# Kernel optimization log

Measured on AMD Instinct MI355X. Metric: run time of the kernel, lower is better.

Reference implementation:

```python
import jax, jax.numpy as jnp
import numpy as np

L = 2        # NUM_DECODER_LAYERS
D = 512      # D_MODEL == ENCODER_EMBEDDING_DIM == DECODER_EMBEDDING_DIM == DECODER_HIDDEN_DIM
T = 32       # max_trg_len (greedy decode steps)
SOS = 1      # SPECIAL_TOKENS.index('[SOS]'), PAD assumed 0


def setup_inputs() -> dict:
    key = jax.random.key(0)
    ks = jax.random.split(key, 12)
    Vin, Vout, B, S = 32000, 32000, 32, 512
    s = 0.02
    src = jax.random.randint(ks[0], (B, S), 0, Vin)
    src_emb_table = jax.random.normal(ks[1], (Vin, D), dtype=jnp.float32) * s
    trg_emb_table = (jax.random.normal(ks[2], (Vout, D), dtype=jnp.float32) * s).at[0].set(0.0)  # padding_idx=0
    Wih = jax.random.normal(ks[3], (L, 4 * D, D), dtype=jnp.float32) * s
    Whh = jax.random.normal(ks[4], (L, 4 * D, D), dtype=jnp.float32) * s
    bih = jnp.zeros((L, 4 * D), jnp.float32)
    bhh = jnp.zeros((L, 4 * D), jnp.float32)
    Wfc = jax.random.normal(ks[5], (D, D), dtype=jnp.float32) * s      # Decoder.fc_out (hid_dim -> hid_dim)
    bfc = jnp.zeros((D,), jnp.float32)
    Wh2o = jax.random.normal(ks[6], (D, 2 * D), dtype=jnp.float32) * s  # hidden_to_out
    bh2o = jnp.zeros((D,), jnp.float32)
    bout = jnp.zeros((Vout,), jnp.float32)                              # out_layer bias (weight tied to trg_emb_table)
    return dict(src=src, src_emb_table=src_emb_table, trg_emb_table=trg_emb_table,
                Wih=Wih, Whh=Whh, bih=bih, bhh=bhh, Wfc=Wfc, bfc=bfc,
                Wh2o=Wh2o, bh2o=bh2o, bout=bout)


def reference(src, src_emb_table, trg_emb_table, Wih, Whh, bih, bhh, Wfc, bfc, Wh2o, bh2o, bout):
    B, S = src.shape
    dtype = src_emb_table.dtype
    scale = jnp.asarray(D ** 0.5, dtype)
    src_e = src_emb_table[src]  # [B,S,D] -- encoder LSTM hidden/cell are computed but discarded in the original

    def lstm_cell(x, h, c, l):
        g = x @ Wih[l].T + bih[l] + h @ Whh[l].T + bhh[l]
        i, f, gg, o = jnp.split(g, 4, axis=-1)  # torch gate order i,f,g,o
        c2 = jax.nn.sigmoid(f) * c + jax.nn.sigmoid(i) * jnp.tanh(gg)
        h2 = jax.nn.sigmoid(o) * jnp.tanh(c2)
        return h2, c2

    def outer_step(carry, t):
        # Original re-runs the decoder LSTM over the whole generated prefix every
        # step, starting from the carried hidden state; we mask positions > t.
        tokens, h, c = carry  # tokens [B,T+1] int32, h/c [L,B,D]
        emb = jnp.swapaxes(trg_emb_table[tokens[:, :T]], 0, 1)  # [T,B,D]

        def pos_step(hc, inp):
            h, c = hc
            x, pos = inp
            active = pos <= t
            hs, cs = [], []
            for l in range(L):
                h2, c2 = lstm_cell(x, h[l], c[l], l)
                h2 = jnp.where(active, h2, h[l])
                c2 = jnp.where(active, c2, c[l])
                hs.append(h2); cs.append(c2)
                x = h2
            h, c = jnp.stack(hs), jnp.stack(cs)
            return (h, c), h[-1]

        (h, c), h_top = jax.lax.scan(pos_step, (h, c), (emb, jnp.arange(T)))
        out_seq = h_top @ Wfc.T + bfc                 # [T,B,D] Decoder.fc_out
        out_t = jnp.take(out_seq, t, axis=0)          # last valid position (concat[:, -1])
        w = jax.nn.softmax(jnp.einsum('bd,bsd->bs', out_t, src_e) / scale, axis=-1)
        context = jnp.einsum('bs,bsd->bd', w, src_e)
        hid = jax.nn.relu(jnp.concatenate([out_t, context], axis=-1) @ Wh2o.T + bh2o)
        logits = hid @ trg_emb_table.T + bout         # out_layer tied to decoder embedding
        nxt = jnp.argmax(logits, axis=-1).astype(tokens.dtype)
        tokens = tokens.at[:, t + 1].set(nxt)
        return (tokens, h, c), out_seq

    tokens0 = jnp.zeros((B, T + 1), jnp.int32).at[:, 0].set(SOS)
    h0 = jnp.zeros((L, B, D), dtype)
    (tokens, _, _), out_seqs = jax.lax.scan(outer_step, (tokens0, h0, h0), jnp.arange(T))
    # attn returned by the original is from the LAST decode step, queries = all T positions
    attn = jax.nn.softmax(jnp.einsum('tbd,bsd->bts', out_seqs[-1], src_e) / scale, axis=-1)  # [B,T,S]
    return tokens[:, 1:], attn
```

## Files before the change

kernel.cpp:

```cpp
#include <hip/hip_runtime.h>
#include <math.h>

#define NWG 256
#define TPB 512
#define AGT __HIP_MEMORY_SCOPE_AGENT

static constexpr int Bb = 32, Dd = 512, Tt = 32, Vv = 32000;
static constexpr int BD = Bb * Dd;
static constexpr float SCALE_INV = 0.04419417382415922f;

static constexpr size_t OFF_H0 = 8192;
static constexpr size_t OFF_H1 = OFF_H0 + 2 * (size_t)BD;
static constexpr size_t OFF_P  = OFF_H1 + 2 * (size_t)BD;
static constexpr size_t OFF_HL = OFF_P + (size_t)Tt * Bb * 2048;
static constexpr size_t OFF_HD = OFF_HL + (size_t)Tt * BD;
static constexpr size_t OFF_OF = OFF_HD + BD;
static constexpr size_t OFF_CV = OFF_OF + (size_t)Tt * BD;
static constexpr size_t OFF_CI = OFF_CV + 32 * 256;
static constexpr size_t OFF_ET = OFF_CI + 32 * 256;

static constexpr int L_W   = 0;
static constexpr int L_ST  = 13824;
static constexpr int L_SC  = 13824;
static constexpr int L_RB  = 14336;
static constexpr int L_IB  = 15360;
static constexpr int L_RED = 15872;
static constexpr int L_HB  = 30208;
static constexpr int L_GV  = 32256;
static constexpr int L_GI  = 32512;
static constexpr int L_TOK = 32768;
static constexpr int LDS_FLOATS = 32800;
static constexpr size_t LDS_BYTES = (size_t)LDS_FLOATS * 4;

__device__ __forceinline__ float sigm(float x) { return 1.0f / (1.0f + expf(-x)); }

__device__ __forceinline__ float ldcv(const float* p) {
  unsigned u = __hip_atomic_load((const unsigned*)p, __ATOMIC_RELAXED, AGT);
  return __builtin_bit_cast(float, u);
}
__device__ __forceinline__ void stcv(float* p, float v) {
  __hip_atomic_store((unsigned*)p, __builtin_bit_cast(unsigned, v), __ATOMIC_RELAXED, AGT);
}
__device__ __forceinline__ float2 ldcv2(const float* p) {
  unsigned long long u = __hip_atomic_load((const unsigned long long*)p, __ATOMIC_RELAXED, AGT);
  return __builtin_bit_cast(float2, u);
}
__device__ __forceinline__ void stcv2(float* p, float2 v) {
  __hip_atomic_store((unsigned long long*)p, __builtin_bit_cast(unsigned long long, v),
                     __ATOMIC_RELAXED, AGT);
}
__device__ __forceinline__ int ldcvi(const int* p) {
  return (int)__hip_atomic_load((const unsigned*)p, __ATOMIC_RELAXED, AGT);
}
__device__ __forceinline__ void stcvi(int* p, int v) {
  __hip_atomic_store((unsigned*)p, (unsigned)v, __ATOMIC_RELAXED, AGT);
}

__device__ __forceinline__ float wredsum(float v) {
#pragma unroll
  for (int off = 32; off > 0; off >>= 1) v += __shfl_xor(v, off, 64);
  return v;
}

__device__ __forceinline__ float rowReduce16(float x) {
  int t;
  t = __builtin_amdgcn_update_dpp(0, __builtin_bit_cast(int, x), 0x121, 0xF, 0xF, false);
  x += __builtin_bit_cast(float, t);
  t = __builtin_amdgcn_update_dpp(0, __builtin_bit_cast(int, x), 0x122, 0xF, 0xF, false);
  x += __builtin_bit_cast(float, t);
  t = __builtin_amdgcn_update_dpp(0, __builtin_bit_cast(int, x), 0x124, 0xF, 0xF, false);
  x += __builtin_bit_cast(float, t);
  t = __builtin_amdgcn_update_dpp(0, __builtin_bit_cast(int, x), 0x128, 0xF, 0xF, false);
  x += __builtin_bit_cast(float, t);
  return x;
}

__device__ __forceinline__ int swzH(int byte) { return byte ^ (((byte >> 8) & 7) << 4); }

__device__ __forceinline__ void gbar(unsigned* sb, unsigned& lg) {
  const unsigned tgt = lg + 1u;
  asm volatile("s_waitcnt vmcnt(0)" ::: "memory");
  __syncthreads();
  const int wg = (int)blockIdx.x;
  if (threadIdx.x < 64) {
    const int lane = (int)threadIdx.x;
    if (lane == 0)
      __hip_atomic_store(&sb[wg * 16], tgt, __ATOMIC_RELAXED, AGT);
    const int g = wg >> 5;
    if ((wg & 31) == 0) {
      if (lane < 32) {
        const unsigned* slot = &sb[(g * 32 + lane) * 16];
        while (__hip_atomic_load(slot, __ATOMIC_RELAXED, AGT) < tgt)
          __builtin_amdgcn_s_sleep(1);
      }
      if (lane == 0)
        __hip_atomic_store(&sb[4096 + g * 16], tgt, __ATOMIC_RELAXED, AGT);
    }
    if (lane < 8) {
      const unsigned* f = &sb[4096 + lane * 16];
      while (__hip_atomic_load(f, __ATOMIC_RELAXED, AGT) < tgt)
        __builtin_amdgcn_s_sleep(1);
// ... 6 lines not shown
__device__ __forceinline__ float blockMax(float v, float* red, int tid) {
#pragma unroll
  for (int off = 32; off > 0; off >>= 1) v = fmaxf(v, __shfl_xor(v, off, 64));
  if ((tid & 63) == 0) red[tid >> 6] = v;
  __syncthreads();
  float m = red[0];
#pragma unroll
  for (int i = 1; i < 8; ++i) m = fmaxf(m, red[i]);
  __syncthreads();
  return m;
}

__device__ __forceinline__ float blockSum(float v, float* red, int tid) {
  v = wredsum(v);
  if ((tid & 63) == 0) red[tid >> 6] = v;
  __syncthreads();
  float s = 0.f;
#pragma unroll
  for (int i = 0; i < 8; ++i) s += red[i];
  __syncthreads();
  return s;
}

__device__ void stageW(int wg, int tid, const float* __restrict__ Wih,
                       const float* __restrict__ Whh, float* __restrict__ SMW) {
  for (int e = tid; e < 24 * 512; e += TPB) {
    const int k = e & 511, rr = e >> 9;
    const int m = rr >> 3, q = (rr >> 1) & 3, dl = rr & 1;
    const int j = q * 512 + wg * 2 + dl;
    const float* srcp = (m == 0) ? (Whh + (size_t)j * 512)
                     : (m == 1) ? (Wih + (size_t)2048 * 512 + (size_t)j * 512)
                                : (Whh + (size_t)2048 * 512 + (size_t)j * 512);
    SMW[rr * 576 + (k >> 5) * 36 + (k & 31)] = srcp[k];
  }
  __syncthreads();
}

__device__ void buildETb(int wg, int tid, const float* __restrict__ Etrg,
                         float* __restrict__ ETb, float* __restrict__ SM) {
  if (wg < 250) {
    for (int tile = 0; tile < 8; ++tile) {
      const int tv = tile >> 2, tk = tile & 3;
      __syncthreads();
      for (int e = tid; e < 64 * 128; e += TPB) {
        const int vl = e >> 7, kl = e & 127;
        SM[vl * 129 + kl] = Etrg[(size_t)(wg * 128 + tv * 64 + vl) * 512 + tk * 128 + kl];
      }
      __syncthreads();
      for (int e = tid; e < 32 * 128; e += TPB) {
        const int vp = e >> 7, kl = e & 127;
        const int v = wg * 128 + tv * 64 + vp * 2;
        const int k = tk * 128 + kl;
        float2 val = make_float2(SM[(vp * 2) * 129 + kl], SM[(vp * 2 + 1) * 129 + kl]);
        stcv2(ETb + ((size_t)(v >> 1) * 512 + k) * 2, val);
      }
    }
    __syncthreads();
  }
}

__device__ __forceinline__ void dotMQ(const float* __restrict__ SMW, int rr, int kc,
                                      const float4* __restrict__ hq, float2& acc) {
  const float4* wr = (const float4*)(SMW + rr * 576 + kc * 36);
#pragma unroll
  for (int i2 = 0; i2 < 8; ++i2) {
    const float4 wv = wr[i2];
    const float4 hA = hq[i2 * 2], hB = hq[i2 * 2 + 1];
    acc.x = fmaf(wv.x, hA.x, acc.x); acc.y = fmaf(wv.x, hA.y, acc.y);
    acc.x = fmaf(wv.y, hA.z, acc.x); acc.y = fmaf(wv.y, hA.w, acc.y);
    acc.x = fmaf(wv.z, hB.x, acc.x); acc.y = fmaf(wv.z, hB.y, acc.y);
    acc.x = fmaf(wv.w, hB.z, acc.x); acc.y = fmaf(wv.w, hB.w, acc.y);
  }
}

__device__ __forceinline__ void phaseAB(
    int wg, int tid, bool doA, bool doB,
    const float* __restrict__ H0r, float* __restrict__ H0w,
    const float* __restrict__ H1r, float* __restrict__ H1w,
    float* __restrict__ HlP, const float* __restrict__ Pp,
    const float* __restrict__ bs1v,
    const float* __restrict__ SMW, float* __restrict__ LH, float* c0, float* c1)
{
  const int b2 = tid >> 5, dl = (tid >> 4) & 1, kc = tid & 15;
  char* LHc = (char*)LH;
  float4 s0[8], s1[8];
  __builtin_amdgcn_sched_barrier(0);
  {
    const float* p0 = H0r + tid * 4;
#pragma unroll
    for (int r = 0; r < 8; ++r)
      asm volatile("global_load_dwordx4 %0, %1, off sc1" : "=v"(s0[r]) : "v"(p0 + r * 2048));
  }
  if (doB) {
    const float* p1 = H1r + tid * 4;
#pragma unroll
    for (int r = 0; r < 8; ++r)
      asm volatile("global_load_dwordx4 %0, %1, off sc1" : "=v"(s1[r]) : "v"(p1 + r * 2048));
    asm volatile("s_waitcnt vmcnt(8)" ::: "memory");
  } else {
    asm volatile("s_waitcnt vmcnt(0)" ::: "memory");
  }
  __builtin_amdgcn_sched_barrier(0);
#pragma unroll
  for (int r = 0; r < 8; ++r)
    *(float4*)(LHc + swzH((r * 512 + tid) * 16)) = s0[r];
  __syncthreads();
  float4 hq[16];
#pragma unroll
  for (int i = 0; i < 16; ++i)
    hq[i] = *(const float4*)(LHc + swzH(b2 * 4096 + kc * 256 + i * 16));

  float2 acc2[12];
#pragma unroll
  for (int j = 0; j < 12; ++j) acc2[j] = make_float2(0.f, 0.f);

  if (doA) {
#pragma unroll
    for (int q = 0; q < 4; ++q) dotMQ(SMW, q * 2 + dl, kc, hq, acc2[q]);
  }
  if (doB) {
#pragma unroll
    for (int q = 0; q < 4; ++q) dotMQ(SMW, 8 + q * 2 + dl, kc, hq, acc2[4 + q]);
    asm volatile("s_waitcnt vmcnt(0)" ::: "memory");
    __builtin_amdgcn_sched_barrier(0);
    __syncthreads();
#pragma unroll
    for (int r = 0; r < 8; ++r)
      *(float4*)(LHc + swzH((r * 512 + tid) * 16)) = s1[r];
    __syncthreads();
#pragma unroll
    for (int i = 0; i < 16; ++i)
      hq[i] = *(const float4*)(LHc + swzH(b2 * 4096 + kc * 256 + i * 16));
#pragma unroll
    for (int q = 0; q < 4; ++q) dotMQ(SMW, 16 + q * 2 + dl, kc, hq, acc2[8 + q]);
  }

#pragma unroll
  for (int j = 0; j < 12; ++j) {
    if (j < 4 ? !doA : !doB) continue;
    acc2[j].x = rowReduce16(acc2[j].x);
    acc2[j].y = rowReduce16(acc2[j].y);
  }

  if (kc == 0) {
    const int d = (wg << 1) | dl;
    if (doA) {
#pragma unroll
      for (int p = 0; p < 2; ++p) {
        const int b = b2 * 2 + p;
        const float* pb = Pp + b * 2048 + d;
        const float gi = (p ? acc2[0].y : acc2[0].x) + pb[0];
        const float gf = (p ? acc2[1].y : acc2[1].x) + pb[512];
        const float gg = (p ? acc2[2].y : acc2[2].x) + pb[1024];
        const float go = (p ? acc2[3].y : acc2[3].x) + pb[1536];
        c0[p] = sigm(gf) * c0[p] + sigm(gi) * tanhf(gg);
        stcv(H0w + b2 * 1024 + d * 2 + p, sigm(go) * tanhf(c0[p]));
      }
    }
    if (doB) {
#pragma unroll
      for (int p = 0; p < 2; ++p) {
        const float gi = (p ? acc2[4].y : acc2[4].x) + (p ? acc2[8].y  : acc2[8].x)  + bs1v[0];
        const float gf = (p ? acc2[5].y : acc2[5].x) + (p ? acc2[9].y  : acc2[9].x)  + bs1v[1];
        const float gg = (p ? acc2[6].y : acc2[6].x) + (p ? acc2[10].y : acc2[10].x) + bs1v[2];
        const float go = (p ? acc2[7].y : acc2[7].x) + (p ? acc2[11].y : acc2[11].x) + bs1v[3];
        c1[p] = sigm(gf) * c1[p] + sigm(gi) * tanhf(gg);
        const float hn = sigm(go) * tanhf(c1[p]);
        stcv(H1w + b2 * 1024 + d * 2 + p, hn);
        if (HlP) stcv(HlP + b2 * 1024 + d * 2 + p, hn);
      }
    }
  }
}

__device__ void phaseCDEF(int b, int tid, const float* __restrict__ H1c,
                          const float* __restrict__ Wfc, const float* __restrict__ bfc,
                          const int* __restrict__ src, const float* __restrict__ Esrc,
                          const float* __restrict__ Wh2o, const float* __restrict__ bh2o,
                          float* __restrict__ hD, float* sc, float* rb, int* ib, float* red)
{
  rb[tid] = ldcv(H1c + (b >> 1) * 1024 + tid * 2 + (b & 1));
  ib[tid] = src[b * 512 + tid];
  __syncthreads();
  const int w = tid >> 6, lane = tid & 63;
  for (int d = w; d < 512; d += 8) {
    const float* wr = Wfc + (size_t)d * 512;
    float p = 0.f;
#pragma unroll
    for (int i = 0; i < 8; ++i) p = fmaf(rb[lane * 8 + i], wr[lane * 8 + i], p);
    p = wredsum(p);
    if (lane == 0) rb[512 + d] = p + bfc[d];
  }
// ... 7 lines not shown
    if (lane == 0) sc[s] = p * SCALE_INV;
  }
  __syncthreads();
  const float mx = blockMax(sc[tid], red, tid);
  const float e = expf(sc[tid] - mx);
  sc[tid] = e;
  const float sum = blockSum(e, red, tid);
  const float inv = 1.0f / sum;
  float acc = 0.f;
#pragma unroll 4
  for (int s = 0; s < 512; ++s) acc = fmaf(sc[s], Esrc[(size_t)ib[s] * 512 + tid], acc);
  rb[tid] = acc * inv;
  __syncthreads();
  for (int d = w; d < 512; d += 8) {
    const float* wr = Wh2o + (size_t)d * 1024;
    float p = 0.f;
#pragma unroll
    for (int i = 0; i < 8; ++i) p = fmaf(rb[512 + lane * 8 + i], wr[lane * 8 + i], p);
#pragma unroll
    for (int i = 0; i < 8; ++i) p = fmaf(rb[lane * 8 + i], wr[512 + lane * 8 + i], p);
    p = wredsum(p);
    if (lane == 0) stcv(hD + (size_t)b * 512 + d, fmaxf(p + bh2o[d], 0.f));
  }
}

__device__ void phaseG(int wg, int tid, int chunk, float* __restrict__ accG,
                       const float* __restrict__ hD, const float* __restrict__ ETb,
                       const float* __restrict__ bout, float* __restrict__ candV,
                       int* __restrict__ candI, float* __restrict__ hblk,
                       float* __restrict__ gv, int* __restrict__ gi)
{
  if (wg >= 250) return;
  if (chunk == 0) {
#pragma unroll
    for (int j = 0; j < 8; ++j) accG[j] = 0.f;
  }
  const int vp = tid >> 3, bh = tid & 7;
  const int v0 = wg * 128 + vp * 2;
  const float* ep = ETb + (size_t)(v0 >> 1) * 1024 + chunk * 512;
  const int fk = tid & 63, fb0 = tid >> 6;
  char* hb = (char*)hblk;

  for (int blk = 0; blk < 4; ++blk) {
    const int kb = chunk * 256 + blk * 64;
    __syncthreads();
#pragma unroll
    for (int i = 0; i < 4; ++i) {
      const int b = fb0 + i * 8;
      const float hv = ldcv(hD + (size_t)b * 512 + kb + fk);
      const int byte = fk * 128 + (((b >> 2) * 16) ^ ((fk & 7) << 4)) + ((b & 3) << 2);
      *(float*)(hb + byte) = hv;
    }
    __syncthreads();
#pragma unroll 8
    for (int kk = 0; kk < 64; kk += 2) {
      const float4 e4 = *(const float4*)ep; ep += 4;
      const float4 ha = *(const float4*)(hb + kk * 128 + ((bh * 16) ^ ((kk & 7) << 4)));
      const float4 hbv = *(const float4*)(hb + (kk + 1) * 128 + ((bh * 16) ^ (((kk + 1) & 7) << 4)));
      accG[0] = fmaf(e4.x, ha.x, accG[0]);  accG[4] = fmaf(e4.y, ha.x, accG[4]);
      accG[1] = fmaf(e4.x, ha.y, accG[1]);  accG[5] = fmaf(e4.y, ha.y, accG[5]);
      accG[2] = fmaf(e4.x, ha.z, accG[2]);  accG[6] = fmaf(e4.y, ha.z, accG[6]);
      accG[3] = fmaf(e4.x, ha.w, accG[3]);  accG[7] = fmaf(e4.y, ha.w, accG[7]);
      accG[0] = fmaf(e4.z, hbv.x, accG[0]); accG[4] = fmaf(e4.w, hbv.x, accG[4]);
      accG[1] = fmaf(e4.z, hbv.y, accG[1]); accG[5] = fmaf(e4.w, hbv.y, accG[5]);
      accG[2] = fmaf(e4.z, hbv.z, accG[2]); accG[6] = fmaf(e4.w, hbv.z, accG[6]);
      accG[3] = fmaf(e4.z, hbv.w, accG[3]); accG[7] = fmaf(e4.w, hbv.w, accG[7]);
    }
  }

  if (chunk == 1) {
    const float bo0 = bout[v0], bo1 = bout[v0 + 1];
    const int w = tid >> 6;
#pragma unroll
    for (int j = 0; j < 4; ++j) {
      const float va = accG[j] + bo0, vb = accG[4 + j] + bo1;
      float bv; int bi;
      if (vb > va) { bv = vb; bi = v0 + 1; } else { bv = va; bi = v0; }
#pragma unroll
      for (int off = 8; off < 64; off <<= 1) {
        const float ov = __shfl_xor(bv, off, 64); const int oi = __shfl_xor(bi, off, 64);
        if (ov > bv || (ov == bv && oi < bi)) { bv = ov; bi = oi; }
      }
      if ((tid & 63) < 8) {
        gv[(bh * 4 + j) * 8 + w] = bv;
        gi[(bh * 4 + j) * 8 + w] = bi;
      }
    }
    __syncthreads();
    if (tid < 32) {
      float bv = -INFINITY; int bi = 0;
      for (int w2 = 0; w2 < 8; ++w2) {
        const float vv = gv[tid * 8 + w2]; const int ii = gi[tid * 8 + w2];
        if (vv > bv || (vv == bv && ii < bi)) { bv = vv; bi = ii; }
      }
      stcv(candV + (size_t)tid * 256 + wg, bv);
      stcvi(candI + tid * 256 + wg, bi);
    }
    __syncthreads();
  }
}

__device__ void phaseG_noET(int wg, int tid, const float* __restrict__ hD,
                            const float* __restrict__ Etrg, const float* __restrict__ bout,
                            float* __restrict__ candV, int* __restrict__ candI,
                            float* rb, float* gv, int* gi)
{
  const int b = wg >> 3, vb = wg & 7;
  rb[tid] = ldcv(hD + (size_t)b * 512 + tid);
  __syncthreads();
  const int w = tid >> 6, lane = tid & 63;
  float bv = -INFINITY; int bi = 0;
  for (int v = vb * 4000 + w; v < (vb + 1) * 4000; v += 8) {
    const float* er = Etrg + (size_t)v * 512;
    float p = 0.f;
#pragma unroll
    for (int i = 0; i < 8; ++i) p = fmaf(rb[lane * 8 + i], er[lane * 8 + i], p);
    p = wredsum(p);
    p += bout[v];
    if (p > bv || (p == bv && v < bi)) { bv = p; bi = v; }
  }
  if (lane == 0) { gv[w] = bv; gi[w] = bi; }
  __syncthreads();
  if (tid == 0) {
    float fv = -INFINITY; int fi = 0;
    for (int w2 = 0; w2 < 8; ++w2)
      if (gv[w2] > fv || (gv[w2] == fv && gi[w2] < fi)) { fv = gv[w2]; fi = gi[w2]; }
    stcv(candV + (size_t)b * 256 + vb, fv);
    stcvi(candI + b * 256 + vb, fi);
  }
  __syncthreads();
}

__device__ void phaseHP(int wg, int tid, int t, bool useET,
                        const float* __restrict__ candV, const int* __restrict__ candI,
                        const float* __restrict__ Etrg, const float* __restrict__ Wih,
                        const float* __restrict__ bih, const float* __restrict__ bhh,
                        float* __restrict__ P, float* __restrict__ out, int* tokL)
{
  const int nslot = useET ? 250 : 8;
  {
    const int b = tid >> 4, sl = tid & 15;
    float bv = -INFINITY; int bi = 0x7fffffff;
    for (int s = sl; s < nslot; s += 16) {
      const float vv = ldcv(candV + (size_t)b * 256 + s);
      const int ii = ldcvi(candI + b * 256 + s);
      if (vv > bv || (vv == bv && ii < bi)) { bv = vv; bi = ii; }
    }
#pragma unroll
    for (int off = 1; off < 16; off <<= 1) {
      const float ov = __shfl_xor(bv, off, 64); const int oi = __shfl_xor(bi, off, 64);
      if (ov > bv || (ov == bv && oi < bi)) { bv = ov; bi = oi; }
    }
    if (sl == 0) {
      tokL[b] = bi;
      if (wg == 0) stcv(out + b * 32 + t, (float)bi);
    }
  }
  __syncthreads();
  if (t < 31) {
    const int w = tid >> 6, lane = tid & 63;
    const int q = w >> 1, dl = w & 1;
    const int j = q * 512 + wg * 2 + dl;
    const float* wr = Wih + (size_t)j * 512;
    const float bsum = bih[j] + bhh[j];
    for (int b = 0; b < 32; ++b) {
      const float* er = Etrg + (size_t)tokL[b] * 512;
      float p = 0.f;
#pragma unroll
      for (int i = 0; i < 8; ++i) p = fmaf(er[lane * 8 + i], wr[lane * 8 + i], p);
      p = wredsum(p);
      if (lane == 0) stcv(P + ((size_t)(t + 1) * 32 + b) * 2048 + j, p + bsum);
    }
  }
  __syncthreads();
}

__device__ void phaseX(int wg, int tid, const float* __restrict__ Hl, const float* __restrict__ Wfc,
                       const float* __restrict__ bfc, float* __restrict__ oF)
{
  const int p = wg >> 3, bq = wg & 7;
  const int w = tid >> 6, lane = tid & 63;
  for (int u = w; u < 1024; u += 8) {
    const int b2 = bq * 2 + (u >> 9), d = u & 511;
    const float* hr = Hl + (size_t)p * BD + b2 * 1024;
    const float* wr = Wfc + (size_t)d * 512;
    float ax = 0.f, ay = 0.f;
#pragma unroll
    for (int i = 0; i < 8; ++i) {
      const float2 hv = ldcv2(hr + (lane * 8 + i) * 2);
      const float wv = wr[lane * 8 + i];
      ax = fmaf(hv.x, wv, ax);
      ay = fmaf(hv.y, wv, ay);
    }
    ax = wredsum(ax); ay = wredsum(ay);
// ... 23 lines not shown
      for (int i = 0; i < 8; ++i) acc = fmaf(rb[lane * 8 + i], er[lane * 8 + i], acc);
      acc = wredsum(acc);
      if (lane == 0) sc[s] = acc * SCALE_INV;
    }
    __syncthreads();
    const float mx = blockMax(sc[tid], red, tid);
    const float e = expf(sc[tid] - mx);
    const float sum = blockSum(e, red, tid);
    out[1024 + ((size_t)b * 32 + p) * 512 + tid] = e / sum;
  }
}

extern "C" __global__ void __launch_bounds__(TPB)
s2s_mega(const int* __restrict__ src, const float* __restrict__ Esrc, const float* __restrict__ Etrg,
         const float* __restrict__ Wih, const float* __restrict__ Whh,
         const float* __restrict__ bih, const float* __restrict__ bhh,
         const float* __restrict__ Wfc, const float* __restrict__ bfc,
         const float* __restrict__ Wh2o, const float* __restrict__ bh2o,
         const float* __restrict__ bout, float* __restrict__ out,
         float* __restrict__ ws, const float* __restrict__ ET, float* __restrict__ ETw)
{
  extern __shared__ float SM[];
  float* SMW = SM + L_W;
  float* LH  = SM + L_ST;
  float* sc  = SM + L_SC;
  float* rb  = SM + L_RB;
  int*   ib  = (int*)(SM + L_IB);
  float* red = SM + L_RED;
  float* hblk = SM + L_HB;
  float* gv  = SM + L_GV;
  int*   gi  = (int*)(SM + L_GI);
  int*   tokL = (int*)(SM + L_TOK);

  unsigned* sb = (unsigned*)ws;
  float* H0 = ws + OFF_H0;
  float* H1 = ws + OFF_H1;
  float* P  = ws + OFF_P;
  float* Hl = ws + OFF_HL;
  float* hD = ws + OFF_HD;
  float* oF = ws + OFF_OF;
  float* cV = ws + OFF_CV;
  int*   cI = (int*)(ws + OFF_CI);

  const int wg = blockIdx.x, tid = threadIdx.x;
  const bool useET = (ET != nullptr);
  unsigned lg = 0u;
  float c0[2] = {0.f, 0.f}, c1[2] = {0.f, 0.f};
  float accG[8];

  float bs1v[4];
  {
    const int dl = (tid >> 4) & 1;
    const int d = (wg << 1) | dl;
#pragma unroll
    for (int q = 0; q < 4; ++q)
      bs1v[q] = bih[2048 + q * 512 + d] + bhh[2048 + q * 512 + d];
  }

  {
    const int gid = wg * TPB + tid;
    if (gid < BD) stcv(H0 + gid, 0.f);
    else if (gid < 2 * BD) stcv(H1 + gid - BD, 0.f);
  }
  {
    const int w = tid >> 6, lane = tid & 63;
    const int q = w >> 1, dl = w & 1;
    const int j = q * 512 + wg * 2 + dl;
    const float* er = Etrg + 512;
    const float* wr = Wih + (size_t)j * 512;
    float p = 0.f;
#pragma unroll
    for (int i = 0; i < 8; ++i) p = fmaf(er[lane * 8 + i], wr[lane * 8 + i], p);
    p = wredsum(p);
    p += bih[j] + bhh[j];
    if (lane < 32) stcv(P + (size_t)lane * 2048 + j, p);
  }
  if (ETw) buildETb(wg, tid, Etrg, ETw, LH);
  stageW(wg, tid, Wih, Whh, SMW);
  gbar(sb, lg);

  int cur0 = 0, cur1 = 0;
  for (int t = 0; t < 32; ++t) {
    for (int k = 0; k <= t + 1; ++k) {
      const bool doA = (k <= t), doB = (k >= 1);
      float* HlP = (t == 31 && doB) ? (Hl + (size_t)(k - 1) * BD) : nullptr;
      const int kp = (k < 32) ? k : 31;
      phaseAB(wg, tid, doA, doB,
              H0 + (size_t)cur0 * BD, H0 + (size_t)(cur0 ^ 1) * BD,
              H1 + (size_t)cur1 * BD, H1 + (size_t)(cur1 ^ 1) * BD,
              HlP, P + (size_t)kp * Bb * 2048, bs1v, SMW, LH, c0, c1);
      if (useET) {
        if (t >= 2 && k == 0) {
          phaseG(wg, tid, 0, accG, hD, ET, bout, cV, cI, hblk, gv, gi);
          if (t == 2) phaseG(wg, tid, 1, accG, hD, ET, bout, cV, cI, hblk, gv, gi);
        }
        if (t >= 3 && k == 1)
          phaseG(wg, tid, 1, accG, hD, ET, bout, cV, cI, hblk, gv, gi);
        if (t == 2 && k == 1)
          phaseHP(wg, tid, 1, true, cV, cI, Etrg, Wih, bih, bhh, P, out, tokL);
        if (t >= 3 && k == 2)
          phaseHP(wg, tid, t - 1, true, cV, cI, Etrg, Wih, bih, bhh, P, out, tokL);
      } else {
        if (t >= 2 && k == 0)
          phaseG_noET(wg, tid, hD, Etrg, bout, cV, cI, hblk, gv, gi);
        if (t >= 2 && k == 1)
          phaseHP(wg, tid, t - 1, false, cV, cI, Etrg, Wih, bih, bhh, P, out, tokL);
      }
      gbar(sb, lg);
      if (doA) cur0 ^= 1;
      if (doB) cur1 ^= 1;
    }
    if (wg < 32) phaseCDEF(wg, tid, H1 + (size_t)cur1 * BD, Wfc, bfc, src, Esrc,
                           Wh2o, bh2o, hD, sc, rb, ib, red);
    gbar(sb, lg);
    if (t == 0) {
      if (useET) {
        phaseG(wg, tid, 0, accG, hD, ET, bout, cV, cI, hblk, gv, gi);
        phaseG(wg, tid, 1, accG, hD, ET, bout, cV, cI, hblk, gv, gi);
      } else {
        phaseG_noET(wg, tid, hD, Etrg, bout, cV, cI, hblk, gv, gi);
      }
      gbar(sb, lg);
      phaseHP(wg, tid, 0, useET, cV, cI, Etrg, Wih, bih, bhh, P, out, tokL);
      gbar(sb, lg);
    }
  }
  phaseX(wg, tid, Hl, Wfc, bfc, oF);
  if (useET) {
    phaseG(wg, tid, 0, accG, hD, ET, bout, cV, cI, hblk, gv, gi);
    phaseG(wg, tid, 1, accG, hD, ET, bout, cV, cI, hblk, gv, gi);
  } else {
    phaseG_noET(wg, tid, hD, Etrg, bout, cV, cI, hblk, gv, gi);
  }
  gbar(sb, lg);
  phaseHP(wg, tid, 31, useET, cV, cI, Etrg, Wih, bih, bhh, P, out, tokL);
  phaseY(wg, tid, oF, src, Esrc, out, sc, rb, ib, red);
}

extern "C" void kernel_launch(void* const* d_in, const int* in_sizes, int n_in,
                              void* d_out, int out_size, void* d_ws, size_t ws_size,
                              hipStream_t stream) {
  const int*   src  = (const int*)d_in[0];
  const float* Esrc = (const float*)d_in[1];
  const float* Etrg = (const float*)d_in[2];
  const float* Wih  = (const float*)d_in[3];
  const float* Whh  = (const float*)d_in[4];
  const float* bih  = (const float*)d_in[5];
  const float* bhh  = (const float*)d_in[6];
  const float* Wfc  = (const float*)d_in[7];
  const float* bfc  = (const float*)d_in[8];
  const float* Wh2o = (const float*)d_in[9];
  const float* bh2o = (const float*)d_in[10];
  const float* bout = (const float*)d_in[11];
  float* ws = (float*)d_ws;

  const size_t needET = (OFF_ET + (size_t)512 * 32000) * sizeof(float);
  const bool useET = (ws_size >= needET);
  float* etw = useET ? (ws + OFF_ET) : nullptr;

// ... 10 lines not shown
```

Baseline: 18.06 ms.

## Split persistent workgroups into LSTM and vocab-projection groups running concurrently

The 256 persistent workgroups are split into two groups. The first 128 run the stacked LSTM recurrence, each now owning 4 hidden units with twice the staged weights in LDS. The other 128 run the tied vocabulary projection, argmax and next-token input projection, so these overlap with the recurrence instead of sharing the same workgroups. Loading of the hidden state into LDS is pipelined in quarter chunks, and the vocab GEMM uses a 4x4 register tile. The LSTM groups now do twice the work per step along the critical path, and LDS regions are reshuffled to fit the new layout.

```diff
diff --git a/kernel.cpp b/kernel.cpp
--- a/kernel.cpp
+++ b/kernel.cpp
@@ -20,17 +20,17 @@
 static constexpr size_t OFF_ET = OFF_CI + 32 * 256;
 
 static constexpr int L_W   = 0;
-static constexpr int L_ST  = 13824;
-static constexpr int L_SC  = 13824;
-static constexpr int L_RB  = 14336;
-static constexpr int L_IB  = 15360;
-static constexpr int L_RED = 15872;
-static constexpr int L_HB  = 30208;
-static constexpr int L_GV  = 32256;
-static constexpr int L_GI  = 32512;
-static constexpr int L_TOK = 32768;
-static constexpr int LDS_FLOATS = 32800;
+static constexpr int L_H   = 27648;
+static constexpr int LDS_FLOATS = 31744;
 static constexpr size_t LDS_BYTES = (size_t)LDS_FLOATS * 4;
+static constexpr int G_HB  = 0;
+static constexpr int G_GV  = 2048;
+static constexpr int G_GI  = 2304;
+static constexpr int G_TOK = 2560;
+static constexpr int S_SC  = L_H;
+static constexpr int S_RB  = L_H + 512;
+static constexpr int S_IB  = L_H + 1536;
+static constexpr int S_RED = L_H + 2048;
 
 __device__ __forceinline__ float sigm(float x) { return 1.0f / (1.0f + expf(-x)); }
 
@@ -75,8 +75,6 @@
   return x;
 }
 
-__device__ __forceinline__ int swzH(int byte) { return byte ^ (((byte >> 8) & 7) << 4); }
-
 __device__ __forceinline__ void gbar(unsigned* sb, unsigned& lg) {
   const unsigned tgt = lg + 1u;
   asm volatile("s_waitcnt vmcnt(0)" ::: "memory");
@@ -129,12 +127,12 @@
   return s;
 }
 
-__device__ void stageW(int wg, int tid, const float* __restrict__ Wih,
-                       const float* __restrict__ Whh, float* __restrict__ SMW) {
-  for (int e = tid; e < 24 * 512; e += TPB) {
+__device__ void stageW4(int wg, int tid, const float* __restrict__ Wih,
+                        const float* __restrict__ Whh, float* __restrict__ SMW) {
+  for (int e = tid; e < 48 * 512; e += TPB) {
     const int k = e & 511, rr = e >> 9;
-    const int m = rr >> 3, q = (rr >> 1) & 3, dl = rr & 1;
-    const int j = q * 512 + wg * 2 + dl;
+    const int m = rr >> 4, q = (rr >> 2) & 3, dl = rr & 3;
+    const int j = q * 512 + wg * 4 + dl;
     const float* srcp = (m == 0) ? (Whh + (size_t)j * 512)
                      : (m == 1) ? (Wih + (size_t)2048 * 512 + (size_t)j * 512)
                                 : (Whh + (size_t)2048 * 512 + (size_t)j * 512);
@@ -166,6 +164,26 @@
   }
 }
 
+__device__ __forceinline__ void ld2q(const float* base, int tid, float4 s[2]) {
+  const float* p0 = base + tid * 4;
+  const float* p1 = base + 2048 + tid * 4;
+  asm volatile("global_load_dwordx4 %0, %1, off sc1" : "=v"(s[0]) : "v"(p0));
+  asm volatile("global_load_dwordx4 %0, %1, off sc1" : "=v"(s[1]) : "v"(p1));
+}
+__device__ __forceinline__ void stage2(char* LHc, int tid, const float4 s[2]) {
+  int byA = tid * 16;         byA ^= ((byA >> 8) & 7) << 4;
+  int byB = (512 + tid) * 16; byB ^= ((byB >> 8) & 7) << 4;
+  *(float4*)(LHc + byA) = s[0];
+  *(float4*)(LHc + byB) = s[1];
+}
+__device__ __forceinline__ void readHq4(const char* LHc, int b2l, int kc, float4 hq[16]) {
+#pragma unroll
+  for (int i = 0; i < 16; ++i) {
+    int byte = b2l * 4096 + kc * 256 + i * 16;
+    byte ^= ((byte >> 8) & 7) << 4;
+    hq[i] = *(const float4*)(LHc + byte);
+  }
+}
 __device__ __forceinline__ void dotMQ(const float* __restrict__ SMW, int rr, int kc,
                                       const float4* __restrict__ hq, float2& acc) {
   const float4* wr = (const float4*)(SMW + rr * 576 + kc * 36);
@@ -180,101 +198,106 @@
   }
 }
 
-__device__ __forceinline__ void phaseAB(
+__device__ __forceinline__ void phaseAB4(
     int wg, int tid, bool doA, bool doB,
     const float* __restrict__ H0r, float* __restrict__ H0w,
     const float* __restrict__ H1r, float* __restrict__ H1w,
     float* __restrict__ HlP, const float* __restrict__ Pp,
-    const float* __restrict__ bs1v,
-    const float* __restrict__ SMW, float* __restrict__ LH, float* c0, float* c1)
+    const float bs1v[2][4], const float* __restrict__ SMW, float* __restrict__ LH,
+    float c0[2][2], float c1[2][2])
 {
-  const int b2 = tid >> 5, dl = (tid >> 4) & 1, kc = tid & 15;
+  const int b2 = tid >> 5, dh = (tid >> 4) & 1, kc = tid & 15;
+  const int q4 = b2 >> 2, b2l = b2 & 3;
   char* LHc = (char*)LH;
-  float4 s0[8], s1[8];
-  __builtin_amdgcn_sched_barrier(0);
-  {
-    const float* p0 = H0r + tid * 4;
-#pragma unroll
-    for (int r = 0; r < 8; ++r)
-      asm volatile("global_load_dwordx4 %0, %1, off sc1" : "=v"(s0[r]) : "v"(p0 + r * 2048));
-  }
-  if (doB) {
-    const float* p1 = H1r + tid * 4;
-#pragma unroll
-    for (int r = 0; r < 8; ++r)
-      asm volatile("global_load_dwordx4 %0, %1, off sc1" : "=v"(s1[r]) : "v"(p1 + r * 2048));
-    asm volatile("s_waitcnt vmcnt(8)" ::: "memory");
-  } else {
-    asm volatile("s_waitcnt vmcnt(0)" ::: "memory");
-  }
-  __builtin_amdgcn_sched_barrier(0);
-#pragma unroll
-  for (int r = 0; r < 8; ++r)
-    *(float4*)(LHc + swzH((r * 512 + tid) * 16)) = s0[r];
-  __syncthreads();
-  float4 hq[16];
-#pragma unroll
-  for (int i = 0; i < 16; ++i)
-    hq[i] = *(const float4*)(LHc + swzH(b2 * 4096 + kc * 256 + i * 16));
-
-  float2 acc2[12];
-#pragma unroll
-  for (int j = 0; j < 12; ++j) acc2[j] = make_float2(0.f, 0.f);
-
-  if (doA) {
-#pragma unroll
-    for (int q = 0; q < 4; ++q) dotMQ(SMW, q * 2 + dl, kc, hq, acc2[q]);
-  }
-  if (doB) {
-#pragma unroll
-    for (int q = 0; q < 4; ++q) dotMQ(SMW, 8 + q * 2 + dl, kc, hq, acc2[4 + q]);
+  float4 s[2], hq[16];
+
+  ld2q(H0r, tid, s);
+#pragma unroll
+  for (int qq = 0; qq < 4; ++qq) {
     asm volatile("s_waitcnt vmcnt(0)" ::: "memory");
     __builtin_amdgcn_sched_barrier(0);
-    __syncthreads();
-#pragma unroll
-    for (int r = 0; r < 8; ++r)
-      *(float4*)(LHc + swzH((r * 512 + tid) * 16)) = s1[r];
-    __syncthreads();
-#pragma unroll
-    for (int i = 0; i < 16; ++i)
-      hq[i] = *(const float4*)(LHc + swzH(b2 * 4096 + kc * 256 + i * 16));
-#pragma unroll
-    for (int q = 0; q < 4; ++q) dotMQ(SMW, 16 + q * 2 + dl, kc, hq, acc2[8 + q]);
-  }
-
-#pragma unroll
-  for (int j = 0; j < 12; ++j) {
-    if (j < 4 ? !doA : !doB) continue;
-    acc2[j].x = rowReduce16(acc2[j].x);
-    acc2[j].y = rowReduce16(acc2[j].y);
-  }
+    stage2(LHc, tid, s);
+    if (qq < 3) ld2q(H0r + (qq + 1) * 4096, tid, s);
+    else if (doB) ld2q(H1r, tid, s);
+    __syncthreads();
+    if (q4 == qq) readHq4(LHc, b2l, kc, hq);
+    __syncthreads();
+  }
+
+  float2 a2[2][12];
+#pragma unroll
+  for (int dlx = 0; dlx < 2; ++dlx)
+#pragma unroll
+    for (int j = 0; j < 12; ++j) a2[dlx][j] = make_float2(0.f, 0.f);
+
+  if (doA) {
+#pragma unroll
+    for (int dlx = 0; dlx < 2; ++dlx)
+#pragma unroll
+      for (int q = 0; q < 4; ++q)
+        dotMQ(SMW, q * 4 + dh * 2 + dlx, kc, hq, a2[dlx][q]);
+  }
+  if (doB) {
+#pragma unroll
+    for (int dlx = 0; dlx < 2; ++dlx)
+#pragma unroll
+      for (int q = 0; q < 4; ++q)
+        dotMQ(SMW, 16 + q * 4 + dh * 2 + dlx, kc, hq, a2[dlx][4 + q]);
+#pragma unroll
+    for (int qq = 0; qq < 4; ++qq) {
+      asm volatile("s_waitcnt vmcnt(0)" ::: "memory");
+      __builtin_amdgcn_sched_barrier(0);
+      stage2(LHc, tid, s);
+      if (qq < 3) ld2q(H1r + (qq + 1) * 4096, tid, s);
+      __syncthreads();
+      if (q4 == qq) readHq4(LHc, b2l, kc, hq);
+      __syncthreads();
+    }
+#pragma unroll
+    for (int dlx = 0; dlx < 2; ++dlx)
+#pragma unroll
+      for (int q = 0; q < 4; ++q)
+        dotMQ(SMW, 32 + q * 4 + dh * 2 + dlx, kc, hq, a2[dlx][8 + q]);
+  }
+
+#pragma unroll
+  for (int dlx = 0; dlx < 2; ++dlx)
+#pragma unroll
+    for (int j = 0; j < 12; ++j) {
+      if (j < 4 ? !doA : !doB) continue;
+      a2[dlx][j].x = rowReduce16(a2[dlx][j].x);
+      a2[dlx][j].y = rowReduce16(a2[dlx][j].y);
+    }
 
   if (kc == 0) {
-    const int d = (wg << 1) | dl;
-    if (doA) {
-#pragma unroll
-      for (int p = 0; p < 2; ++p) {
-        const int b = b2 * 2 + p;
-        const float* pb = Pp + b * 2048 + d;
-        const float gi = (p ? acc2[0].y : acc2[0].x) + pb[0];
-        const float gf = (p ? acc2[1].y : acc2[1].x) + pb[512];
-        const float gg = (p ? acc2[2].y : acc2[2].x) + pb[1024];
-        const float go = (p ? acc2[3].y : acc2[3].x) + pb[1536];
-        c0[p] = sigm(gf) * c0[p] + sigm(gi) * tanhf(gg);
-        stcv(H0w + b2 * 1024 + d * 2 + p, sigm(go) * tanhf(c0[p]));
-      }
-    }
-    if (doB) {
-#pragma unroll
-      for (int p = 0; p < 2; ++p) {
-        const float gi = (p ? acc2[4].y : acc2[4].x) + (p ? acc2[8].y  : acc2[8].x)  + bs1v[0];
-        const float gf = (p ? acc2[5].y : acc2[5].x) + (p ? acc2[9].y  : acc2[9].x)  + bs1v[1];
-        const float gg = (p ? acc2[6].y : acc2[6].x) + (p ? acc2[10].y : acc2[10].x) + bs1v[2];
-        const float go = (p ? acc2[7].y : acc2[7].x) + (p ? acc2[11].y : acc2[11].x) + bs1v[3];
-        c1[p] = sigm(gf) * c1[p] + sigm(gi) * tanhf(gg);
-        const float hn = sigm(go) * tanhf(c1[p]);
-        stcv(H1w + b2 * 1024 + d * 2 + p, hn);
-        if (HlP) stcv(HlP + b2 * 1024 + d * 2 + p, hn);
+#pragma unroll
+    for (int dlx = 0; dlx < 2; ++dlx) {
+      const int d = (wg << 2) | (dh << 1) | dlx;
+      if (doA) {
+#pragma unroll
+        for (int p = 0; p < 2; ++p) {
+          const int b = b2 * 2 + p;
+          const float* pb = Pp + b * 2048 + d;
+          const float gi = (p ? a2[dlx][0].y : a2[dlx][0].x) + pb[0];
+          const float gf = (p ? a2[dlx][1].y : a2[dlx][1].x) + pb[512];
+          const float gg = (p ? a2[dlx][2].y : a2[dlx][2].x) + pb[1024];
+          const float go = (p ? a2[dlx][3].y : a2[dlx][3].x) + pb[1536];
+          c0[dlx][p] = sigm(gf) * c0[dlx][p] + sigm(gi) * tanhf(gg);
+          stcv(H0w + b2 * 1024 + d * 2 + p, sigm(go) * tanhf(c0[dlx][p]));
+        }
+      }
+      if (doB) {
+#pragma unroll
+        for (int p = 0; p < 2; ++p) {
+          const float gi = (p ? a2[dlx][4].y : a2[dlx][4].x) + (p ? a2[dlx][8].y  : a2[dlx][8].x)  + bs1v[dlx][0];
+          const float gf = (p ? a2[dlx][5].y : a2[dlx][5].x) + (p ? a2[dlx][9].y  : a2[dlx][9].x)  + bs1v[dlx][1];
+          const float gg = (p ? a2[dlx][6].y : a2[dlx][6].x) + (p ? a2[dlx][10].y : a2[dlx][10].x) + bs1v[dlx][2];
+          const float go = (p ? a2[dlx][7].y : a2[dlx][7].x) + (p ? a2[dlx][11].y : a2[dlx][11].x) + bs1v[dlx][3];
+          c1[dlx][p] = sigm(gf) * c1[dlx][p] + sigm(gi) * tanhf(gg);
+          const float hn = sigm(go) * tanhf(c1[dlx][p]);
+          stcv(H1w + b2 * 1024 + d * 2 + p, hn);
+          if (HlP) stcv(HlP + b2 * 1024 + d * 2 + p, hn);
+        }
       }
     }
   }
@@ -328,22 +351,26 @@
     p = wredsum(p);
     if (lane == 0) stcv(hD + (size_t)b * 512 + d, fmaxf(p + bh2o[d], 0.f));
   }
-}
-
-__device__ void phaseG(int wg, int tid, int chunk, float* __restrict__ accG,
-                       const float* __restrict__ hD, const float* __restrict__ ETb,
-                       const float* __restrict__ bout, float* __restrict__ candV,
-                       int* __restrict__ candI, float* __restrict__ hblk,
-                       float* __restrict__ gv, int* __restrict__ gi)
+  __syncthreads();
+}
+
+__device__ void phaseG_panelC(int wgG, int tid, int chunk, float (*acc)[4],
+                              const float* __restrict__ hD, const float* __restrict__ ETb,
+                              const float* __restrict__ bout, float* __restrict__ candV,
+                              int* __restrict__ candI, float* __restrict__ hblk,
+                              float* __restrict__ gv, int* __restrict__ gi)
 {
-  if (wg >= 250) return;
+  if (wgG >= 125) return;
   if (chunk == 0) {
 #pragma unroll
-    for (int j = 0; j < 8; ++j) accG[j] = 0.f;
+    for (int a = 0; a < 4; ++a)
+#pragma unroll
+      for (int b = 0; b < 4; ++b) acc[a][b] = 0.f;
   }
   const int vp = tid >> 3, bh = tid & 7;
-  const int v0 = wg * 128 + vp * 2;
-  const float* ep = ETb + (size_t)(v0 >> 1) * 1024 + chunk * 512;
+  const int v0 = wgG * 256 + vp * 4;
+  const float* epA = ETb + (size_t)(v0 >> 1) * 1024 + chunk * 512;
+  const float* epB = epA + 1024;
   const int fk = tid & 63, fb0 = tid >> 6;
   char* hb = (char*)hblk;
 
@@ -360,36 +387,44 @@
     __syncthreads();
 #pragma unroll 8
     for (int kk = 0; kk < 64; kk += 2) {
-      const float4 e4 = *(const float4*)ep; ep += 4;
-      const float4 ha = *(const float4*)(hb + kk * 128 + ((bh * 16) ^ ((kk & 7) << 4)));
-      const float4 hbv = *(const float4*)(hb + (kk + 1) * 128 + ((bh * 16) ^ (((kk + 1) & 7) << 4)));
-      accG[0] = fmaf(e4.x, ha.x, accG[0]);  accG[4] = fmaf(e4.y, ha.x, accG[4]);
-      accG[1] = fmaf(e4.x, ha.y, accG[1]);  accG[5] = fmaf(e4.y, ha.y, accG[5]);
-      accG[2] = fmaf(e4.x, ha.z, accG[2]);  accG[6] = fmaf(e4.y, ha.z, accG[6]);
-      accG[3] = fmaf(e4.x, ha.w, accG[3]);  accG[7] = fmaf(e4.y, ha.w, accG[7]);
-      accG[0] = fmaf(e4.z, hbv.x, accG[0]); accG[4] = fmaf(e4.w, hbv.x, accG[4]);
-      accG[1] = fmaf(e4.z, hbv.y, accG[1]); accG[5] = fmaf(e4.w, hbv.y, accG[5]);
-      accG[2] = fmaf(e4.z, hbv.z, accG[2]); accG[6] = fmaf(e4.w, hbv.z, accG[6]);
-      accG[3] = fmaf(e4.z, hbv.w, accG[3]); accG[7] = fmaf(e4.w, hbv.w, accG[7]);
-    }
-  }
-
+      const float4 eA = *(const float4*)epA; epA += 4;
+      const float4 eB = *(const float4*)epB; epB += 4;
+      const float4 h0 = *(const float4*)(hb + kk * 128 + ((bh * 16) ^ ((kk & 7) << 4)));
+      const float4 h1 = *(const float4*)(hb + (kk + 1) * 128 + ((bh * 16) ^ (((kk + 1) & 7) << 4)));
+#pragma unroll
+      for (int bj = 0; bj < 4; ++bj) {
+        const float h0v = (bj == 0) ? h0.x : (bj == 1) ? h0.y : (bj == 2) ? h0.z : h0.w;
+        const float h1v = (bj == 0) ? h1.x : (bj == 1) ? h1.y : (bj == 2) ? h1.z : h1.w;
+        acc[0][bj] = fmaf(eA.x, h0v, acc[0][bj]);
+        acc[0][bj] = fmaf(eA.z, h1v, acc[0][bj]);
+        acc[1][bj] = fmaf(eA.y, h0v, acc[1][bj]);
+        acc[1][bj] = fmaf(eA.w, h1v, acc[1][bj]);
+        acc[2][bj] = fmaf(eB.x, h0v, acc[2][bj]);
+        acc[2][bj] = fmaf(eB.z, h1v, acc[2][bj]);
+        acc[3][bj] = fmaf(eB.y, h0v, acc[3][bj]);
+        acc[3][bj] = fmaf(eB.w, h1v, acc[3][bj]);
+      }
+    }
+  }
   if (chunk == 1) {
-    const float bo0 = bout[v0], bo1 = bout[v0 + 1];
+    const float bo[4] = {bout[v0], bout[v0 + 1], bout[v0 + 2], bout[v0 + 3]};
     const int w = tid >> 6;
 #pragma unroll
-    for (int j = 0; j < 4; ++j) {
-      const float va = accG[j] + bo0, vb = accG[4 + j] + bo1;
-      float bv; int bi;
-      if (vb > va) { bv = vb; bi = v0 + 1; } else { bv = va; bi = v0; }
+    for (int bj = 0; bj < 4; ++bj) {
+      float bv = acc[0][bj] + bo[0]; int bi = v0;
+#pragma unroll
+      for (int vj = 1; vj < 4; ++vj) {
+        const float vv = acc[vj][bj] + bo[vj];
+        if (vv > bv) { bv = vv; bi = v0 + vj; }
+      }
 #pragma unroll
       for (int off = 8; off < 64; off <<= 1) {
         const float ov = __shfl_xor(bv, off, 64); const int oi = __shfl_xor(bi, off, 64);
         if (ov > bv || (ov == bv && oi < bi)) { bv = ov; bi = oi; }
       }
       if ((tid & 63) < 8) {
-        gv[(bh * 4 + j) * 8 + w] = bv;
-        gi[(bh * 4 + j) * 8 + w] = bi;
+        gv[(bh * 4 + bj) * 8 + w] = bv;
+        gi[(bh * 4 + bj) * 8 + w] = bi;
       }
     }
     __syncthreads();
@@ -399,51 +434,52 @@
         const float vv = gv[tid * 8 + w2]; const int ii = gi[tid * 8 + w2];
         if (vv > bv || (vv == bv && ii < bi)) { bv = vv; bi = ii; }
       }
-      stcv(candV + (size_t)tid * 256 + wg, bv);
-      stcvi(candI + tid * 256 + wg, bi);
-    }
-    __syncthreads();
-  }
-}
-
-__device__ void phaseG_noET(int wg, int tid, const float* __restrict__ hD,
-                            const float* __restrict__ Etrg, const float* __restrict__ bout,
-                            float* __restrict__ candV, int* __restrict__ candI,
-                            float* rb, float* gv, int* gi)
+      stcv(candV + (size_t)tid * 256 + wgG, bv);
+      stcvi(candI + tid * 256 + wgG, bi);
+    }
+    __syncthreads();
+  }
+}
+
+__device__ void phaseG_noET2(int wgG, int tid, const float* __restrict__ hD,
+                             const float* __restrict__ Etrg, const float* __restrict__ bout,
+                             float* __restrict__ candV, int* __restrict__ candI,
+                             float* rb, float* gv, int* gi)
 {
-  const int b = wg >> 3, vb = wg & 7;
-  rb[tid] = ldcv(hD + (size_t)b * 512 + tid);
-  __syncthreads();
   const int w = tid >> 6, lane = tid & 63;
-  float bv = -INFINITY; int bi = 0;
-  for (int v = vb * 4000 + w; v < (vb + 1) * 4000; v += 8) {
-    const float* er = Etrg + (size_t)v * 512;
-    float p = 0.f;
-#pragma unroll
-    for (int i = 0; i < 8; ++i) p = fmaf(rb[lane * 8 + i], er[lane * 8 + i], p);
-    p = wredsum(p);
-    p += bout[v];
-    if (p > bv || (p == bv && v < bi)) { bv = p; bi = v; }
-  }
-  if (lane == 0) { gv[w] = bv; gi[w] = bi; }
-  __syncthreads();
-  if (tid == 0) {
-    float fv = -INFINITY; int fi = 0;
-    for (int w2 = 0; w2 < 8; ++w2)
-      if (gv[w2] > fv || (gv[w2] == fv && gi[w2] < fi)) { fv = gv[w2]; fi = gi[w2]; }
-    stcv(candV + (size_t)b * 256 + vb, fv);
-    stcvi(candI + b * 256 + vb, fi);
-  }
-  __syncthreads();
-}
-
-__device__ void phaseHP(int wg, int tid, int t, bool useET,
-                        const float* __restrict__ candV, const int* __restrict__ candI,
-                        const float* __restrict__ Etrg, const float* __restrict__ Wih,
-                        const float* __restrict__ bih, const float* __restrict__ bhh,
-                        float* __restrict__ P, float* __restrict__ out, int* tokL)
+  for (int b = 0; b < 32; ++b) {
+    __syncthreads();
+    rb[tid & 511] = ldcv(hD + (size_t)b * 512 + (tid & 511));
+    __syncthreads();
+    float bv = -INFINITY; int bi = 0x7fffffff;
+    for (int v = wgG * 250 + w; v < wgG * 250 + 250; v += 8) {
+      const float* er = Etrg + (size_t)v * 512;
+      float p = 0.f;
+#pragma unroll
+      for (int i = 0; i < 8; ++i) p = fmaf(rb[lane * 8 + i], er[lane * 8 + i], p);
+      p = wredsum(p);
+      p += bout[v];
+      if (p > bv || (p == bv && v < bi)) { bv = p; bi = v; }
+    }
+    if (lane == 0) { gv[w] = bv; gi[w] = bi; }
+    __syncthreads();
+    if (tid == 0) {
+      float fv = -INFINITY; int fi = 0x7fffffff;
+      for (int w2 = 0; w2 < 8; ++w2)
+        if (gv[w2] > fv || (gv[w2] == fv && gi[w2] < fi)) { fv = gv[w2]; fi = gi[w2]; }
+      stcv(candV + (size_t)b * 256 + wgG, fv);
+      stcvi(candI + b * 256 + wgG, fi);
+    }
+  }
+  __syncthreads();
+}
+
+__device__ void phaseHP_G(int wgG, int tid, int t, int nslot,
+                          const float* __restrict__ candV, const int* __restrict__ candI,
+                          const float* __restrict__ Etrg, const float* __restrict__ Wih,
+                          const float* __restrict__ bih, const float* __restrict__ bhh,
+                          float* __restrict__ P, float* __restrict__ out, int* tokL)
 {
-  const int nslot = useET ? 250 : 8;
   {
     const int b = tid >> 4, sl = tid & 15;
     float bv = -INFINITY; int bi = 0x7fffffff;
@@ -459,23 +495,24 @@
     }
     if (sl == 0) {
       tokL[b] = bi;
-      if (wg == 0) stcv(out + b * 32 + t, (float)bi);
+      if (wgG == 0) stcv(out + b * 32 + t, (float)bi);
     }
   }
   __syncthreads();
   if (t < 31) {
     const int w = tid >> 6, lane = tid & 63;
-    const int q = w >> 1, dl = w & 1;
-    const int j = q * 512 + wg * 2 + dl;
-    const float* wr = Wih + (size_t)j * 512;
-    const float bsum = bih[j] + bhh[j];
-    for (int b = 0; b < 32; ++b) {
-      const float* er = Etrg + (size_t)tokL[b] * 512;
-      float p = 0.f;
-#pragma unroll
-      for (int i = 0; i < 8; ++i) p = fmaf(er[lane * 8 + i], wr[lane * 8 + i], p);
-      p = wredsum(p);
-      if (lane == 0) stcv(P + ((size_t)(t + 1) * 32 + b) * 2048 + j, p + bsum);
+    for (int jj = w; jj < 16; jj += 8) {
+      const int j = wgG * 16 + jj;
+      const float* wr = Wih + (size_t)j * 512;
+      const float bsum = bih[j] + bhh[j];
+      for (int b = 0; b < 32; ++b) {
+        const float* er = Etrg + (size_t)tokL[b] * 512;
+        float p = 0.f;
+#pragma unroll
+        for (int i = 0; i < 8; ++i) p = fmaf(er[lane * 8 + i], wr[lane * 8 + i], p);
+        p = wredsum(p);
+        if (lane == 0) stcv(P + ((size_t)(t + 1) * 32 + b) * 2048 + j, p + bsum);
+      }
     }
   }
   __syncthreads();
@@ -545,15 +582,15 @@
 {
   extern __shared__ float SM[];
   float* SMW = SM + L_W;
-  float* LH  = SM + L_ST;
-  float* sc  = SM + L_SC;
-  float* rb  = SM + L_RB;
-  int*   ib  = (int*)(SM + L_IB);
-  float* red = SM + L_RED;
-  float* hblk = SM + L_HB;
-  float* gv  = SM + L_GV;
-  int*   gi  = (int*)(SM + L_GI);
-  int*   tokL = (int*)(SM + L_TOK);
+  float* LH  = SM + L_H;
+  float* hblk = SM + G_HB;
+  float* gv  = SM + G_GV;
+  int*   gi  = (int*)(SM + G_GI);
+  int*   tokG = (int*)(SM + G_TOK);
+  float* scY = SM + S_SC;
+  float* rbY = SM + S_RB;
+  int*   ibY = (int*)(SM + S_IB);
+  float* redY = SM + S_RED;
 
   unsigned* sb = (unsigned*)ws;
   float* H0 = ws + OFF_H0;
@@ -568,16 +605,20 @@
   const int wg = blockIdx.x, tid = threadIdx.x;
   const bool useET = (ET != nullptr);
   unsigned lg = 0u;
-  float c0[2] = {0.f, 0.f}, c1[2] = {0.f, 0.f};
-  float accG[8];
-
-  float bs1v[4];
-  {
-    const int dl = (tid >> 4) & 1;
-    const int d = (wg << 1) | dl;
-#pragma unroll
-    for (int q = 0; q < 4; ++q)
-      bs1v[q] = bih[2048 + q * 512 + d] + bhh[2048 + q * 512 + d];
+  float c0[2][2] = {{0.f, 0.f}, {0.f, 0.f}};
+  float c1[2][2] = {{0.f, 0.f}, {0.f, 0.f}};
+  float accG[4][4];
+  float bs1v[2][4] = {{0.f,0.f,0.f,0.f},{0.f,0.f,0.f,0.f}};
+
+  if (wg < 128) {
+    const int dh = (tid >> 4) & 1;
+#pragma unroll
+    for (int dlx = 0; dlx < 2; ++dlx) {
+      const int d = (wg << 2) | (dh << 1) | dlx;
+#pragma unroll
+      for (int q = 0; q < 4; ++q)
+        bs1v[dlx][q] = bih[2048 + q * 512 + d] + bhh[2048 + q * 512 + d];
+    }
   }
 
   {
@@ -598,66 +639,80 @@
     p += bih[j] + bhh[j];
     if (lane < 32) stcv(P + (size_t)lane * 2048 + j, p);
   }
-  if (ETw) buildETb(wg, tid, Etrg, ETw, LH);
-  stageW(wg, tid, Wih, Whh, SMW);
+  if (ETw) buildETb(wg, tid, Etrg, ETw, SM);
+  if (wg < 128) stageW4(wg, tid, Wih, Whh, SMW);
   gbar(sb, lg);
 
   int cur0 = 0, cur1 = 0;
   for (int t = 0; t < 32; ++t) {
     for (int k = 0; k <= t + 1; ++k) {
       const bool doA = (k <= t), doB = (k >= 1);
-      float* HlP = (t == 31 && doB) ? (Hl + (size_t)(k - 1) * BD) : nullptr;
-      const int kp = (k < 32) ? k : 31;
-      phaseAB(wg, tid, doA, doB,
-              H0 + (size_t)cur0 * BD, H0 + (size_t)(cur0 ^ 1) * BD,
-              H1 + (size_t)cur1 * BD, H1 + (size_t)(cur1 ^ 1) * BD,
-              HlP, P + (size_t)kp * Bb * 2048, bs1v, SMW, LH, c0, c1);
-      if (useET) {
-        if (t >= 2 && k == 0) {
-          phaseG(wg, tid, 0, accG, hD, ET, bout, cV, cI, hblk, gv, gi);
-          if (t == 2) phaseG(wg, tid, 1, accG, hD, ET, bout, cV, cI, hblk, gv, gi);
+      if (wg < 128) {
+        float* HlP = (t == 31 && doB) ? (Hl + (size_t)(k - 1) * BD) : nullptr;
+        const int kp = (k < 32) ? k : 31;
+        phaseAB4(wg, tid, doA, doB,
+                 H0 + (size_t)cur0 * BD, H0 + (size_t)(cur0 ^ 1) * BD,
+                 H1 + (size_t)cur1 * BD, H1 + (size_t)(cur1 ^ 1) * BD,
+                 HlP, P + (size_t)kp * Bb * 2048, bs1v, SMW, LH, c0, c1);
+      } else {
+        const int wgG = wg - 128;
+        if (useET) {
+          if (t >= 2 && k == 0) {
+            phaseG_panelC(wgG, tid, 0, accG, hD, ET, bout, cV, cI, hblk, gv, gi);
+            if (t == 2) phaseG_panelC(wgG, tid, 1, accG, hD, ET, bout, cV, cI, hblk, gv, gi);
+          }
+          if (t >= 3 && k == 1)
+            phaseG_panelC(wgG, tid, 1, accG, hD, ET, bout, cV, cI, hblk, gv, gi);
+          if (t == 2 && k == 1)
+            phaseHP_G(wgG, tid, 1, 125, cV, cI, Etrg, Wih, bih, bhh, P, out, tokG);
+          if (t >= 3 && k == 2)
+            phaseHP_G(wgG, tid, t - 1, 125, cV, cI, Etrg, Wih, bih, bhh, P, out, tokG);
+        } else {
+          if (t >= 2 && k == 0)
+            phaseG_noET2(wgG, tid, hD, Etrg, bout, cV, cI, hblk, gv, gi);
+          if (t == 2 && k == 1)
+            phaseHP_G(wgG, tid, 1, 128, cV, cI, Etrg, Wih, bih, bhh, P, out, tokG);
+          if (t >= 3 && k == 2)
+            phaseHP_G(wgG, tid, t - 1, 128, cV, cI, Etrg, Wih, bih, bhh, P, out, tokG);
         }
-        if (t >= 3 && k == 1)
-          phaseG(wg, tid, 1, accG, hD, ET, bout, cV, cI, hblk, gv, gi);
-        if (t == 2 && k == 1)
-          phaseHP(wg, tid, 1, true, cV, cI, Etrg, Wih, bih, bhh, P, out, tokL);
-        if (t >= 3 && k == 2)
-          phaseHP(wg, tid, t - 1, true, cV, cI, Etrg, Wih, bih, bhh, P, out, tokL);
-      } else {
-        if (t >= 2 && k == 0)
-          phaseG_noET(wg, tid, hD, Etrg, bout, cV, cI, hblk, gv, gi);
-        if (t >= 2 && k == 1)
-          phaseHP(wg, tid, t - 1, false, cV, cI, Etrg, Wih, bih, bhh, P, out, tokL);
       }
       gbar(sb, lg);
       if (doA) cur0 ^= 1;
       if (doB) cur1 ^= 1;
     }
     if (wg < 32) phaseCDEF(wg, tid, H1 + (size_t)cur1 * BD, Wfc, bfc, src, Esrc,
-                           Wh2o, bh2o, hD, sc, rb, ib, red);
+                           Wh2o, bh2o, hD, scY, rbY, ibY, redY);
     gbar(sb, lg);
     if (t == 0) {
-      if (useET) {
-        phaseG(wg, tid, 0, accG, hD, ET, bout, cV, cI, hblk, gv, gi);
-        phaseG(wg, tid, 1, accG, hD, ET, bout, cV, cI, hblk, gv, gi);
-      } else {
-        phaseG_noET(wg, tid, hD, Etrg, bout, cV, cI, hblk, gv, gi);
+      if (wg >= 128) {
+        const int wgG = wg - 128;
+        if (useET) {
+          phaseG_panelC(wgG, tid, 0, accG, hD, ET, bout, cV, cI, hblk, gv, gi);
+          phaseG_panelC(wgG, tid, 1, accG, hD, ET, bout, cV, cI, hblk, gv, gi);
+        } else {
+          phaseG_noET2(wgG, tid, hD, Etrg, bout, cV, cI, hblk, gv, gi);
+        }
       }
       gbar(sb, lg);
-      phaseHP(wg, tid, 0, useET, cV, cI, Etrg, Wih, bih, bhh, P, out, tokL);
+      if (wg >= 128)
+        phaseHP_G(wg - 128, tid, 0, useET ? 125 : 128, cV, cI, Etrg, Wih, bih, bhh, P, out, tokG);
       gbar(sb, lg);
     }
   }
   phaseX(wg, tid, Hl, Wfc, bfc, oF);
-  if (useET) {
-    phaseG(wg, tid, 0, accG, hD, ET, bout, cV, cI, hblk, gv, gi);
-    phaseG(wg, tid, 1, accG, hD, ET, bout, cV, cI, hblk, gv, gi);
-  } else {
-    phaseG_noET(wg, tid, hD, Etrg, bout, cV, cI, hblk, gv, gi);
+  if (wg >= 128) {
+    const int wgG = wg - 128;
+    if (useET) {
+      phaseG_panelC(wgG, tid, 0, accG, hD, ET, bout, cV, cI, hblk, gv, gi);
+      phaseG_panelC(wgG, tid, 1, accG, hD, ET, bout, cV, cI, hblk, gv, gi);
+    } else {
+      phaseG_noET2(wgG, tid, hD, Etrg, bout, cV, cI, hblk, gv, gi);
+    }
   }
   gbar(sb, lg);
-  phaseHP(wg, tid, 31, useET, cV, cI, Etrg, Wih, bih, bhh, P, out, tokL);
-  phaseY(wg, tid, oF, src, Esrc, out, sc, rb, ib, red);
+  if (wg >= 128)
+    phaseHP_G(wg - 128, tid, 31, useET ? 125 : 128, cV, cI, Etrg, Wih, bih, bhh, P, out, tokG);
+  phaseY(wg, tid, oF, src, Esrc, out, scY, rbY, ibY, redY);
 }
 
 extern "C" void kernel_launch(void* const* d_in, const int* in_sizes, int n_in,
```

Measured after the change: 47.79 ms. +164.6%, slower.
